# Kernel tuning notes

Hardware: AMD Instinct MI355X
Metric: run time of the kernel (lower is better)

## Reference

```python
import jax, jax.numpy as jnp
import numpy as np

N_NODES = 50000
N_EDGES = 800000
D = 64


def setup_inputs() -> dict:
    key = jax.random.key(0)
    ks = jax.random.split(key, 8)
    scale = 1.0 / np.sqrt(D)
    x = jax.random.normal(ks[0], (N_NODES, D), dtype=jnp.float32)
    edge_index = jax.random.randint(ks[1], (2, N_EDGES), 0, N_NODES, dtype=jnp.int64)
    W1_root = jax.random.normal(ks[2], (D, D), dtype=jnp.float32) * scale
    W1_nbr = jax.random.normal(ks[3], (D, D), dtype=jnp.float32) * scale
    b1 = jnp.zeros((D,), dtype=jnp.float32)
    W2_root = jax.random.normal(ks[4], (D, D), dtype=jnp.float32) * scale
    W2_nbr = jax.random.normal(ks[5], (D, D), dtype=jnp.float32) * scale
    b2 = jnp.zeros((D,), dtype=jnp.float32)
    return {"x": x, "edge_index": edge_index,
            "W1_root": W1_root, "W1_nbr": W1_nbr, "b1": b1,
            "W2_root": W2_root, "W2_nbr": W2_nbr, "b2": b2}


def graph_conv(x, src, dst, W_root, W_nbr, b, n_nodes):
    # sum-aggregate neighbor features: msg j->i uses x[src], scattered to dst
    agg = jax.ops.segment_sum(x[src], dst, num_segments=n_nodes)  # [N, D]
    return x @ W_root + agg @ W_nbr + b


def reference(x, edge_index, W1_root, W1_nbr, b1, W2_root, W2_nbr, b2):
    src, dst = edge_index[0], edge_index[1]
    n = x.shape[0]
    h = jax.nn.relu(graph_conv(x, src, dst, W1_root, W1_nbr, b1, n))
    out = graph_conv(h, src, dst, W2_root, W2_nbr, b2, n)
    return out
```

## Files before the change

### kernel.cpp

```cpp
#include <hip/hip_runtime.h>

#define N_NODES 50000
#define N_EDGES 800000
#define D 64
#define NBUCKETS 196
#define BCAP 8192
#define SBLOCKS 256
#define CHUNK (N_EDGES / SBLOCKS)
#define CASTBLOCKS 3125

__device__ __forceinline__ unsigned short f2bf(float f) {
    unsigned u = __float_as_uint(f);
    return (unsigned short)((u + 0x7fffu + ((u >> 16) & 1u)) >> 16);
}
__device__ __forceinline__ float bflo(unsigned u) {
    return __uint_as_float(u << 16);
}
__device__ __forceinline__ float bfhi(unsigned u) {
    return __uint_as_float(u & 0xffff0000u);
}

__global__ void __launch_bounds__(256) scatter_cast_kernel(
    const int* __restrict__ src, const int* __restrict__ dst,
    const float* __restrict__ X,
    int* __restrict__ cursorPad, int* __restrict__ staged,
    unsigned short* __restrict__ Xbf) {
    int t = threadIdx.x;
    if (blockIdx.x >= SBLOCKS) {
        int i = (blockIdx.x - SBLOCKS) * 256 + t;
        float4 v = ((const float4*)X)[i];
        ushort4 r;
        r.x = f2bf(v.x); r.y = f2bf(v.y); r.z = f2bf(v.z); r.w = f2bf(v.w);
        ((ushort4*)Xbf)[i] = r;
        return;
    }
    __shared__ int hist[256];
    __shared__ int curs[256];
    hist[t] = 0;
    __syncthreads();
    int lo = blockIdx.x * CHUNK, hi = lo + CHUNK;
    for (int i = lo + t; i < hi; i += 256)
        atomicAdd(&hist[dst[i] >> 8], 1);
    __syncthreads();
    if (hist[t] > 0)
        curs[t] = t * BCAP + atomicAdd(&cursorPad[t * 16], hist[t]);
    __syncthreads();
    for (int i = lo + t; i < hi; i += 256) {
        int d = dst[i];
        int b = d >> 8;
        int pos = atomicAdd(&curs[b], 1);
        staged[pos] = (src[i] << 8) | (d & 255);
    }
}

__global__ void __launch_bounds__(256) csr_build_kernel(
    const int* __restrict__ cursorPad, const int* __restrict__ staged,
    int* __restrict__ csr, int* __restrict__ startA, int* __restrict__ endA) {
    __shared__ int deg[256];
    __shared__ int sc[256];
    __shared__ int curs[256];
    int k = blockIdx.x;
    int t = threadIdx.x;
    int base = k * BCAP;
    int cnt  = cursorPad[k * 16];
    deg[t] = 0;
    __syncthreads();
    for (int i = t; i < cnt; i += 256)
        atomicAdd(&deg[staged[base + i] & 255], 1);
    __syncthreads();
    int v = deg[t];
    sc[t] = v;
    __syncthreads();
#pragma unroll
    for (int d = 1; d < 256; d <<= 1) {
        int u = (t >= d) ? sc[t - d] : 0;
        __syncthreads();
        sc[t] += u;
        __syncthreads();
    }
    int start = sc[t] - v;
    int node = k * 256 + t;
    if (node < N_NODES) {
        startA[node] = base + start;
        endA[node]   = base + start + v;
    }
    curs[t] = start;
    __syncthreads();
    for (int i = t; i < cnt; i += 256) {
        int e = staged[base + i];
        int pos = atomicAdd(&curs[e & 255], 1);
        csr[base + pos] = e >> 8;
    }
}

__global__ void __launch_bounds__(256) gather_bf16(
    const unsigned short* __restrict__ Xbf, const int* __restrict__ startA,
    const int* __restrict__ endA, const int* __restrict__ csr,
    unsigned short* __restrict__ aggbf) {
    int tid = threadIdx.x;
    int wave = tid >> 6, lane = tid & 63;
    int node = blockIdx.x * 4 + wave;
    int sub = lane >> 4, fq = lane & 15;
    int j0 = startA[node], je = endA[node];
    float a0 = 0.f, a1 = 0.f, a2 = 0.f, a3 = 0.f;
    for (int jb = j0; jb < je; jb += 64) {
        int idx = jb + lane;
        int p = csr[idx < je ? idx : (je - 1)];
        int m = min(64, je - jb);
        int b = 0;
        for (; b + 16 <= m; b += 16) {
            int i0 = __shfl(p, b + sub, 64);
            int i1 = __shfl(p, b + 4 + sub, 64);
            int i2 = __shfl(p, b + 8 + sub, 64);
            int i3 = __shfl(p, b + 12 + sub, 64);
            uint2 u0 = *(const uint2*)(Xbf + i0 * D + fq * 4);
            uint2 u1 = *(const uint2*)(Xbf + i1 * D + fq * 4);
            uint2 u2 = *(const uint2*)(Xbf + i2 * D + fq * 4);
            uint2 u3 = *(const uint2*)(Xbf + i3 * D + fq * 4);
            a0 += bflo(u0.x) + bflo(u1.x) + bflo(u2.x) + bflo(u3.x);
            a1 += bfhi(u0.x) + bfhi(u1.x) + bfhi(u2.x) + bfhi(u3.x);
            a2 += bflo(u0.y) + bflo(u1.y) + bflo(u2.y) + bflo(u3.y);
            a3 += bfhi(u0.y) + bfhi(u1.y) + bfhi(u2.y) + bfhi(u3.y);
        }
        for (; b < m; b += 4) {
            int sidx = b + sub;
            int scl = sidx < m ? sidx : (m - 1);
            int i0 = __shfl(p, scl, 64);
            if (sidx < m) {
                uint2 u = *(const uint2*)(Xbf + i0 * D + fq * 4);
                a0 += bflo(u.x); a1 += bfhi(u.x);
                a2 += bflo(u.y); a3 += bfhi(u.y);
            }
        }
    }
#pragma unroll
    for (int mk = 16; mk <= 32; mk <<= 1) {
        a0 += __shfl_xor(a0, mk, 64);
        a1 += __shfl_xor(a1, mk, 64);
        a2 += __shfl_xor(a2, mk, 64);
        a3 += __shfl_xor(a3, mk, 64);
    }
    if (sub == 0) {
        ushort4 r;
        r.x = f2bf(a0); r.y = f2bf(a1); r.z = f2bf(a2); r.w = f2bf(a3);
        *(ushort4*)(aggbf + (size_t)node * D + fq * 4) = r;
    }
}

template<int RELU, int WOUT, int WBF, int XBF>
__global__ void __launch_bounds__(256) dual_gemm(
    const float* __restrict__ Xf, const unsigned short* __restrict__ Xb,
    const unsigned short* __restrict__ Abf,
    const float* __restrict__ Wr, const float* __restrict__ Wn,
    const float* __restrict__ bias, float* __restrict__ out,
    unsigned short* __restrict__ outBf) {
    __shared__ float sXT[D][D];
    __shared__ float sAT[D][D];
    __shared__ float sWr[D][D];
    __shared__ float sWn[D][D];

    int tid = threadIdx.x;
    int node0 = blockIdx.x * 64;

#pragma unroll
    for (int i = 0; i < 4; i++) {
        int idx = tid + 256 * i;
        ((float4*)sWr)[idx] = ((const float4*)Wr)[idx];
        ((float4*)sWn)[idx] = ((const float4*)Wn)[idx];
    }
    int nd = tid & 63;
    int gn = min(node0 + nd, N_NODES - 1);
#pragma unroll
    for (int pass = 0; pass < 2; pass++) {
        int kg = (tid >> 6) + pass * 4;
        int k0 = kg * 8;
        uint4 ua = *(const uint4*)(Abf + (size_t)gn * D + k0);
        sAT[k0 + 0][nd] = bflo(ua.x); sAT[k0 + 1][nd] = bfhi(ua.x);
        sAT[k0 + 2][nd] = bflo(ua.y); sAT[k0 + 3][nd] = bfhi(ua.y);
        sAT[k0 + 4][nd] = bflo(ua.z); sAT[k0 + 5][nd] = bfhi(ua.z);
        sAT[k0 + 6][nd] = bflo(ua.w); sAT[k0 + 7][nd] = bfhi(ua.w);
        if (XBF) {
            uint4 ux = *(const uint4*)(Xb + (size_t)gn * D + k0);
            sXT[k0 + 0][nd] = bflo(ux.x); sXT[k0 + 1][nd] = bfhi(ux.x);
            sXT[k0 + 2][nd] = bflo(ux.y); sXT[k0 + 3][nd] = bfhi(ux.y);
            sXT[k0 + 4][nd] = bflo(ux.z); sXT[k0 + 5][nd] = bfhi(ux.z);
            sXT[k0 + 6][nd] = bflo(ux.w); sXT[k0 + 7][nd] = bfhi(ux.w);
        }
    }
    if (!XBF) {
        const float4* X4 = (const float4*)Xf;
#pragma unroll
        for (int pass = 0; pass < 4; pass++) {
            int kq = (tid >> 6) + pass * 4;
            float4 v = X4[gn * 16 + kq];
            sXT[kq * 4 + 0][nd] = v.x; sXT[kq * 4 + 1][nd] = v.y;
            sXT[kq * 4 + 2][nd] = v.z; sXT[kq * 4 + 3][nd] = v.w;
        }
    }
    __syncthreads();

    int nq = tid >> 4;
    int cq = tid & 15;
    float4 b4 = ((const float4*)bias)[cq];
    float acc[4][4];
#pragma unroll
    for (int i = 0; i < 4; i++) {
        acc[i][0] = b4.x; acc[i][1] = b4.y; acc[i][2] = b4.z; acc[i][3] = b4.w;
    }

#pragma unroll 16
    for (int k = 0; k < D; k++) {
        float4 xv = *(const float4*)&sXT[k][nq * 4];
        float4 av = *(const float4*)&sAT[k][nq * 4];
        float4 wr = *(const float4*)&sWr[k][cq * 4];
        float4 wn = *(const float4*)&sWn[k][cq * 4];
        float xs[4] = {xv.x, xv.y, xv.z, xv.w};
        float as[4] = {av.x, av.y, av.z, av.w};
        float rs[4] = {wr.x, wr.y, wr.z, wr.w};
        float ns[4] = {wn.x, wn.y, wn.z, wn.w};
#pragma unroll
        for (int i = 0; i < 4; i++)
#pragma unroll
            for (int jj = 0; jj < 4; jj++) {
                acc[i][jj] = fmaf(xs[i], rs[jj], acc[i][jj]);
                acc[i][jj] = fmaf(as[i], ns[jj], acc[i][jj]);
            }
    }

    float4* out4 = (float4*)out;
#pragma unroll
    for (int i = 0; i < 4; i++) {
        int node = node0 + nq * 4 + i;
        if (node < N_NODES) {
            float4 r;
            r.x = acc[i][0]; r.y = acc[i][1]; r.z = acc[i][2]; r.w = acc[i][3];
            if (RELU) {
                r.x = fmaxf(r.x, 0.f); r.y = fmaxf(r.y, 0.f);
                r.z = fmaxf(r.z, 0.f); r.w = fmaxf(r.w, 0.f);
            }
            if (WOUT) out4[node * 16 + cq] = r;
            if (WBF) {
                ushort4 rb;
                rb.x = f2bf(r.x); rb.y = f2bf(r.y);
                rb.z = f2bf(r.z); rb.w = f2bf(r.w);
                *(ushort4*)(outBf + (size_t)node * D + cq * 4) = rb;
            }
        }
    }
}

extern "C" void kernel_launch(void* const* d_in, const int* in_sizes, int n_in,
                              void* d_out, int out_size, void* d_ws, size_t ws_size,
                              hipStream_t stream) {
    const float* x   = (const float*)d_in[0];
    const int*   edg = (const int*)d_in[1];
    const float* W1r = (const float*)d_in[2];
    const float* W1n = (const float*)d_in[3];
    const float* b1  = (const float*)d_in[4];
    const float* W2r = (const float*)d_in[5];
    const float* W2n = (const float*)d_in[6];
    const float* b2  = (const float*)d_in[7];
    float* out = (float*)d_out;

    const int* src = edg;
    const int* dst = edg + N_EDGES;

    int* W              = (int*)d_ws;
    int* cursorPad      = W;
    int* staged         = W + 4096;
    int* csr            = staged + NBUCKETS * BCAP;
    int* startA         = csr + NBUCKETS * BCAP;
    int* endA           = startA + N_NODES;
    unsigned short* xbf = (unsigned short*)(endA + N_NODES);
    unsigned short* hbf = xbf + (size_t)N_NODES * D;
    unsigned short* agb = hbf + (size_t)N_NODES * D;

    hipMemsetAsync(cursorPad, 0, 196 * 16 * sizeof(int), stream);
    scatter_cast_kernel<<<SBLOCKS + CASTBLOCKS, 256, 0, stream>>>(
        src, dst, x, cursorPad, staged, xbf);
    csr_build_kernel<<<NBUCKETS, 256, 0, stream>>>(cursorPad, staged, csr,
                                                   startA, endA);

    const int GB = N_NODES / 4;
    const int MB = (N_NODES + 63) / 64;

    gather_bf16<<<GB, 256, 0, stream>>>(xbf, startA, endA, csr, agb);
    dual_gemm<1, 0, 1, 0><<<MB, 256, 0, stream>>>(x, (unsigned short*)0, agb,
                                                  W1r, W1n, b1, out, hbf);
    gather_bf16<<<GB, 256, 0, stream>>>(hbf, startA, endA, csr, agb);
    dual_gemm<0, 1, 0, 1><<<MB, 256, 0, stream>>>((const float*)0, hbf, agb,
                                                  W2r, W2n, b2, out,
                                                  (unsigned short*)0);
}
```

Before: 199.8 us.

## Fuse neighbor gather into dual GEMM and stage edge chunk in LDS

Removes the separate gather kernels: each GEMM block now aggregates its 64 nodes' neighbor features directly into shared memory, avoiding the bf16 aggregate buffer round trip and two launches. The scatter kernel also caches packed edges and bucket ids in LDS so src/dst are read once. The fusion reduces gather parallelism to one wave handling 16 nodes serially in far fewer blocks, which may expose memory latency in the latency-bound gather.

```diff
diff --git a/kernel.cpp b/kernel.cpp
--- a/kernel.cpp
+++ b/kernel.cpp
@@ -36,20 +36,26 @@
     }
     __shared__ int hist[256];
     __shared__ int curs[256];
+    __shared__ int pk[CHUNK];
+    __shared__ unsigned char bk[CHUNK];
     hist[t] = 0;
     __syncthreads();
-    int lo = blockIdx.x * CHUNK, hi = lo + CHUNK;
-    for (int i = lo + t; i < hi; i += 256)
-        atomicAdd(&hist[dst[i] >> 8], 1);
+    int lo = blockIdx.x * CHUNK;
+    for (int i = t; i < CHUNK; i += 256) {
+        int d = dst[lo + i];
+        int s = src[lo + i];
+        pk[i] = (s << 8) | (d & 255);
+        bk[i] = (unsigned char)(d >> 8);
+        atomicAdd(&hist[d >> 8], 1);
+    }
     __syncthreads();
     if (hist[t] > 0)
         curs[t] = t * BCAP + atomicAdd(&cursorPad[t * 16], hist[t]);
     __syncthreads();
-    for (int i = lo + t; i < hi; i += 256) {
-        int d = dst[i];
-        int b = d >> 8;
+    for (int i = t; i < CHUNK; i += 256) {
+        int b = bk[i];
         int pos = atomicAdd(&curs[b], 1);
-        staged[pos] = (src[i] << 8) | (d & 255);
+        staged[pos] = pk[i];
     }
 }
 
@@ -93,64 +99,12 @@
     }
 }
 
-__global__ void __launch_bounds__(256) gather_bf16(
-    const unsigned short* __restrict__ Xbf, const int* __restrict__ startA,
-    const int* __restrict__ endA, const int* __restrict__ csr,
-    unsigned short* __restrict__ aggbf) {
-    int tid = threadIdx.x;
-    int wave = tid >> 6, lane = tid & 63;
-    int node = blockIdx.x * 4 + wave;
-    int sub = lane >> 4, fq = lane & 15;
-    int j0 = startA[node], je = endA[node];
-    float a0 = 0.f, a1 = 0.f, a2 = 0.f, a3 = 0.f;
-    for (int jb = j0; jb < je; jb += 64) {
-        int idx = jb + lane;
-        int p = csr[idx < je ? idx : (je - 1)];
-        int m = min(64, je - jb);
-        int b = 0;
-        for (; b + 16 <= m; b += 16) {
-            int i0 = __shfl(p, b + sub, 64);
-            int i1 = __shfl(p, b + 4 + sub, 64);
-            int i2 = __shfl(p, b + 8 + sub, 64);
-            int i3 = __shfl(p, b + 12 + sub, 64);
-            uint2 u0 = *(const uint2*)(Xbf + i0 * D + fq * 4);
-            uint2 u1 = *(const uint2*)(Xbf + i1 * D + fq * 4);
-            uint2 u2 = *(const uint2*)(Xbf + i2 * D + fq * 4);
-            uint2 u3 = *(const uint2*)(Xbf + i3 * D + fq * 4);
-            a0 += bflo(u0.x) + bflo(u1.x) + bflo(u2.x) + bflo(u3.x);
-            a1 += bfhi(u0.x) + bfhi(u1.x) + bfhi(u2.x) + bfhi(u3.x);
-            a2 += bflo(u0.y) + bflo(u1.y) + bflo(u2.y) + bflo(u3.y);
-            a3 += bfhi(u0.y) + bfhi(u1.y) + bfhi(u2.y) + bfhi(u3.y);
-        }
-        for (; b < m; b += 4) {
-            int sidx = b + sub;
-            int scl = sidx < m ? sidx : (m - 1);
-            int i0 = __shfl(p, scl, 64);
-            if (sidx < m) {
-                uint2 u = *(const uint2*)(Xbf + i0 * D + fq * 4);
-                a0 += bflo(u.x); a1 += bfhi(u.x);
-                a2 += bflo(u.y); a3 += bfhi(u.y);
-            }
-        }
-    }
-#pragma unroll
-    for (int mk = 16; mk <= 32; mk <<= 1) {
-        a0 += __shfl_xor(a0, mk, 64);
-        a1 += __shfl_xor(a1, mk, 64);
-        a2 += __shfl_xor(a2, mk, 64);
-        a3 += __shfl_xor(a3, mk, 64);
-    }
-    if (sub == 0) {
-        ushort4 r;
-        r.x = f2bf(a0); r.y = f2bf(a1); r.z = f2bf(a2); r.w = f2bf(a3);
-        *(ushort4*)(aggbf + (size_t)node * D + fq * 4) = r;
-    }
-}
-
 template<int RELU, int WOUT, int WBF, int XBF>
-__global__ void __launch_bounds__(256) dual_gemm(
+__global__ void __launch_bounds__(256) fused_layer(
     const float* __restrict__ Xf, const unsigned short* __restrict__ Xb,
-    const unsigned short* __restrict__ Abf,
+    const unsigned short* __restrict__ Gsrc,
+    const int* __restrict__ startA, const int* __restrict__ endA,
+    const int* __restrict__ csr,
     const float* __restrict__ Wr, const float* __restrict__ Wn,
     const float* __restrict__ bias, float* __restrict__ out,
     unsigned short* __restrict__ outBf) {
@@ -170,24 +124,18 @@
     }
     int nd = tid & 63;
     int gn = min(node0 + nd, N_NODES - 1);
-#pragma unroll
-    for (int pass = 0; pass < 2; pass++) {
-        int kg = (tid >> 6) + pass * 4;
-        int k0 = kg * 8;
-        uint4 ua = *(const uint4*)(Abf + (size_t)gn * D + k0);
-        sAT[k0 + 0][nd] = bflo(ua.x); sAT[k0 + 1][nd] = bfhi(ua.x);
-        sAT[k0 + 2][nd] = bflo(ua.y); sAT[k0 + 3][nd] = bfhi(ua.y);
-        sAT[k0 + 4][nd] = bflo(ua.z); sAT[k0 + 5][nd] = bfhi(ua.z);
-        sAT[k0 + 6][nd] = bflo(ua.w); sAT[k0 + 7][nd] = bfhi(ua.w);
-        if (XBF) {
+    if (XBF) {
+#pragma unroll
+        for (int pass = 0; pass < 2; pass++) {
+            int kg = (tid >> 6) + pass * 4;
+            int k0 = kg * 8;
             uint4 ux = *(const uint4*)(Xb + (size_t)gn * D + k0);
             sXT[k0 + 0][nd] = bflo(ux.x); sXT[k0 + 1][nd] = bfhi(ux.x);
             sXT[k0 + 2][nd] = bflo(ux.y); sXT[k0 + 3][nd] = bfhi(ux.y);
             sXT[k0 + 4][nd] = bflo(ux.z); sXT[k0 + 5][nd] = bfhi(ux.z);
             sXT[k0 + 6][nd] = bflo(ux.w); sXT[k0 + 7][nd] = bfhi(ux.w);
         }
-    }
-    if (!XBF) {
+    } else {
         const float4* X4 = (const float4*)Xf;
 #pragma unroll
         for (int pass = 0; pass < 4; pass++) {
@@ -195,6 +143,58 @@
             float4 v = X4[gn * 16 + kq];
             sXT[kq * 4 + 0][nd] = v.x; sXT[kq * 4 + 1][nd] = v.y;
             sXT[kq * 4 + 2][nd] = v.z; sXT[kq * 4 + 3][nd] = v.w;
+        }
+    }
+
+    int wave = tid >> 6, lane = tid & 63;
+    int sub = lane >> 4, fq = lane & 15;
+    for (int n = 0; n < 16; ++n) {
+        int c = wave * 16 + n;
+        int node = min(node0 + c, N_NODES - 1);
+        int j0 = startA[node], je = endA[node];
+        float a0 = 0.f, a1 = 0.f, a2 = 0.f, a3 = 0.f;
+        for (int jb = j0; jb < je; jb += 64) {
+            int idx = jb + lane;
+            int p = csr[idx < je ? idx : (je - 1)];
+            int m = min(64, je - jb);
+            int b = 0;
+            for (; b + 16 <= m; b += 16) {
+                int i0 = __shfl(p, b + sub, 64);
+                int i1 = __shfl(p, b + 4 + sub, 64);
+                int i2 = __shfl(p, b + 8 + sub, 64);
+                int i3 = __shfl(p, b + 12 + sub, 64);
+                uint2 u0 = *(const uint2*)(Gsrc + i0 * D + fq * 4);
+                uint2 u1 = *(const uint2*)(Gsrc + i1 * D + fq * 4);
+                uint2 u2 = *(const uint2*)(Gsrc + i2 * D + fq * 4);
+                uint2 u3 = *(const uint2*)(Gsrc + i3 * D + fq * 4);
+                a0 += bflo(u0.x) + bflo(u1.x) + bflo(u2.x) + bflo(u3.x);
+                a1 += bfhi(u0.x) + bfhi(u1.x) + bfhi(u2.x) + bfhi(u3.x);
+                a2 += bflo(u0.y) + bflo(u1.y) + bflo(u2.y) + bflo(u3.y);
+                a3 += bfhi(u0.y) + bfhi(u1.y) + bfhi(u2.y) + bfhi(u3.y);
+            }
+            for (; b < m; b += 4) {
+                int sidx = b + sub;
+                int scl = sidx < m ? sidx : (m - 1);
+                int i0 = __shfl(p, scl, 64);
+                if (sidx < m) {
+                    uint2 u = *(const uint2*)(Gsrc + i0 * D + fq * 4);
+                    a0 += bflo(u.x); a1 += bfhi(u.x);
+                    a2 += bflo(u.y); a3 += bfhi(u.y);
+                }
+            }
+        }
+#pragma unroll
+        for (int mk = 16; mk <= 32; mk <<= 1) {
+            a0 += __shfl_xor(a0, mk, 64);
+            a1 += __shfl_xor(a1, mk, 64);
+            a2 += __shfl_xor(a2, mk, 64);
+            a3 += __shfl_xor(a3, mk, 64);
+        }
+        if (sub == 0) {
+            sAT[fq * 4 + 0][c] = a0;
+            sAT[fq * 4 + 1][c] = a1;
+            sAT[fq * 4 + 2][c] = a2;
+            sAT[fq * 4 + 3][c] = a3;
         }
     }
     __syncthreads();
@@ -273,7 +273,6 @@
     int* endA           = startA + N_NODES;
     unsigned short* xbf = (unsigned short*)(endA + N_NODES);
     unsigned short* hbf = xbf + (size_t)N_NODES * D;
-    unsigned short* agb = hbf + (size_t)N_NODES * D;
 
     hipMemsetAsync(cursorPad, 0, 196 * 16 * sizeof(int), stream);
     scatter_cast_kernel<<<SBLOCKS + CASTBLOCKS, 256, 0, stream>>>(
@@ -281,14 +280,12 @@
     csr_build_kernel<<<NBUCKETS, 256, 0, stream>>>(cursorPad, staged, csr,
                                                    startA, endA);
 
-    const int GB = N_NODES / 4;
     const int MB = (N_NODES + 63) / 64;
 
-    gather_bf16<<<GB, 256, 0, stream>>>(xbf, startA, endA, csr, agb);
-    dual_gemm<1, 0, 1, 0><<<MB, 256, 0, stream>>>(x, (unsigned short*)0, agb,
-                                                  W1r, W1n, b1, out, hbf);
-    gather_bf16<<<GB, 256, 0, stream>>>(hbf, startA, endA, csr, agb);
-    dual_gemm<0, 1, 0, 1><<<MB, 256, 0, stream>>>((const float*)0, hbf, agb,
-                                                  W2r, W2n, b2, out,
-                                                  (unsigned short*)0);
-}
+    fused_layer<1, 0, 1, 0><<<MB, 256, 0, stream>>>(
+        x, (const unsigned short*)0, xbf, startA, endA, csr,
+        W1r, W1n, b1, out, hbf);
+    fused_layer<0, 1, 0, 1><<<MB, 256, 0, stream>>>(
+        (const float*)0, hbf, hbf, startA, endA, csr,
+        W2r, W2n, b2, out, (unsigned short*)0);
+}
```

Result: slower. 359.9 us (+80.1%).
